# Optimization experiments

Measured on AMD Instinct MI355X. Metric: run time of the kernel, lower is better.

Reference implementation:

```python
import jax, jax.numpy as jnp
import numpy as np

EMBED_DIM = 1024
NUM_HEADS = 16
HEAD_DIM = EMBED_DIM // NUM_HEADS
NUM_FEATS = 256
YAT_EPS = 0.1
BATCH = 4
SEQ = 4096


def setup_inputs() -> dict:
    key = jax.random.key(0)
    ks = jax.random.split(key, 6)
    s = 1.0 / np.sqrt(EMBED_DIM)
    return {
        "x": jax.random.normal(ks[0], (BATCH, SEQ, EMBED_DIM), jnp.float32),
        "Wq": jax.random.normal(ks[1], (EMBED_DIM, EMBED_DIM), jnp.float32) * s,
        "bq": jnp.zeros((EMBED_DIM,), jnp.float32),
        "Wk": jax.random.normal(ks[2], (EMBED_DIM, EMBED_DIM), jnp.float32) * s,
        "bk": jnp.zeros((EMBED_DIM,), jnp.float32),
        "Wv": jax.random.normal(ks[3], (EMBED_DIM, EMBED_DIM), jnp.float32) * s,
        "bv": jnp.zeros((EMBED_DIM,), jnp.float32),
        "Wo": jax.random.normal(ks[4], (EMBED_DIM, EMBED_DIM), jnp.float32) * s,
        "bo": jnp.zeros((EMBED_DIM,), jnp.float32),
        "projection": jax.random.normal(ks[5], (NUM_HEADS, NUM_FEATS, HEAD_DIM), jnp.float32),
    }


def _spherical_features(x, projection):
    # x: (b, h, s, d) -> (b, h, s, f)
    x_norm = x / (jnp.linalg.norm(x, axis=-1, keepdims=True) + 1e-8)
    proj = jnp.einsum('bhsd,hfd->bhsf', x_norm, projection)
    return jax.nn.relu(proj) + YAT_EPS


def reference(x, Wq, bq, Wk, bk, Wv, bv, Wo, bo, projection):
    b, s, _ = x.shape
    def heads(t):
        return jnp.transpose(t.reshape(b, s, NUM_HEADS, HEAD_DIM), (0, 2, 1, 3))
    Q = heads(x @ Wq + bq)
    K = heads(x @ Wk + bk)
    V = heads(x @ Wv + bv)
    Qp = _spherical_features(Q, projection)  # (b,h,s,f)
    Kp = _spherical_features(K, projection)
    KV = jnp.einsum('bhsf,bhsd->bhfd', Kp, V)           # (b,h,f,d)
    QKV = jnp.einsum('bhsf,bhfd->bhsd', Qp, KV)          # (b,h,s,d)
    K_sum = jnp.sum(Kp, axis=2)                          # (b,h,f)
    normalizer = jnp.einsum('bhsf,bhf->bhs', Qp, K_sum)[..., None]
    normalizer = jnp.maximum(normalizer, 1e-6)
    out = QKV / normalizer
    out = jnp.transpose(out, (0, 2, 1, 3)).reshape(b, s, EMBED_DIM)
    return out @ Wo + bo
```

## Files before the change

### kernel.cpp

```cpp
#include <hip/hip_runtime.h>
#include <stdint.h>

typedef __bf16 bf16_t;
typedef __bf16 bf16x4 __attribute__((ext_vector_type(4)));
typedef __bf16 bf16x8 __attribute__((ext_vector_type(8)));
typedef float  f32x4  __attribute__((ext_vector_type(4)));

typedef __attribute__((address_space(1))) const uint32_t gas_u32;
typedef __attribute__((address_space(3))) uint32_t las_u32;

#define MFMA16(a, b, c) __builtin_amdgcn_mfma_f32_16x16x32_bf16((a), (b), (c), 0, 0, 0)
#define SBAR() __builtin_amdgcn_s_barrier()
#define WAIT_LGKM0() asm volatile("s_waitcnt lgkmcnt(0)")

__device__ __forceinline__ void gl_lds16(const bf16_t* g, bf16_t* l) {
    __builtin_amdgcn_global_load_lds((gas_u32*)g, (las_u32*)l, 16, 0, 0);
}

__global__ __launch_bounds__(256) void castbf(const float* __restrict__ X,
                                              bf16_t* __restrict__ Xb)
{
    size_t i = ((size_t)blockIdx.x * 256 + threadIdx.x) * 8;
    float4 a = *(const float4*)&X[i];
    float4 b = *(const float4*)&X[i + 4];
    bf16x8 o;
    o[0] = (bf16_t)a.x; o[1] = (bf16_t)a.y; o[2] = (bf16_t)a.z; o[3] = (bf16_t)a.w;
    o[4] = (bf16_t)b.x; o[5] = (bf16_t)b.y; o[6] = (bf16_t)b.z; o[7] = (bf16_t)b.w;
    *(bf16x8*)&Xb[i] = o;
}

__global__ __launch_bounds__(256) void ktrans(
    const float* __restrict__ W0, const float* __restrict__ W1,
    const float* __restrict__ W2, const float* __restrict__ W3,
    bf16_t* __restrict__ WT)
{
    __shared__ float t[64 * 68];
    const int z = blockIdx.z;
    const float* W = (z == 0) ? W0 : (z == 1) ? W1 : (z == 2) ? W2 : W3;
    bf16_t* O = WT + (size_t)z * 1024 * 1024;
    const int r0 = blockIdx.y * 64, c0 = blockIdx.x * 64;
    const int tid = threadIdx.x;
    const int row = tid >> 2, colg = (tid & 3) * 16;
#pragma unroll
    for (int p = 0; p < 4; ++p)
        *(float4*)&t[row * 68 + colg + p * 4] =
            *(const float4*)&W[(size_t)(r0 + row) * 1024 + c0 + colg + p * 4];
    __syncthreads();
    bf16x8 v0, v1;
#pragma unroll
    for (int j = 0; j < 8; ++j) {
        v0[j] = (bf16_t)t[(colg + j) * 68 + row];
        v1[j] = (bf16_t)t[(colg + 8 + j) * 68 + row];
    }
    *(bf16x8*)&O[(size_t)(c0 + row) * 1024 + r0 + colg] = v0;
    *(bf16x8*)&O[(size_t)(c0 + row) * 1024 + r0 + colg + 8] = v1;
}

template <int CMODE, typename OutT>
__global__ __launch_bounds__(512, 2) void gemm256(
    const bf16_t* __restrict__ A, const bf16_t* __restrict__ Bt,
    const float* __restrict__ b0, const float* __restrict__ b1,
    const float* __restrict__ b2, OutT* __restrict__ C,
    int M, int N, int K)
{
    __shared__ bf16_t lds[2][2][256 * 64];
    const int tid = threadIdx.x;
    const int lane = tid & 63, wave = tid >> 6;
    const int q = lane >> 4, ln = lane & 15;
    const int m0 = blockIdx.x * 256, n0 = blockIdx.y * 256;
    const int wm = (wave >> 2) * 128, wn = (wave & 3) * 64;
    const int NT = K >> 6;

    const bf16_t* Ag = A + (size_t)m0 * K;
    const bf16_t* Bg = Bt + (size_t)n0 * K;

    const bf16_t* gstage[4][2];
    bf16_t* lstage[4][2];
#pragma unroll
    for (int cs = 0; cs < 4; ++cs) {
        const int mat = cs >> 1, half = cs & 1;
#pragma unroll
        for (int r = 0; r < 2; ++r) {
            int idx = r * 512 + tid;
            int ri = idx >> 3;
            int row = mat ? (half * 32 + (ri & 31) + ((ri & ~31) << 1))
                          : (half * 64 + (ri & 63) + ((ri & 64) << 1));
            int gs = (idx & 7) ^ (row & 7);
            gstage[cs][r] = (mat ? Bg : Ag) + (size_t)row * K + gs * 8;
            lstage[cs][r] = &lds[0][mat][row * 64 + (idx & 7) * 8];
        }
    }
    auto stage = [&](int cs, int tt) {
        const int koff = tt << 6;
        const int bsel = (tt & 1) << 15;
#pragma unroll
        for (int r = 0; r < 2; ++r)
            gl_lds16(gstage[cs][r] + koff, lstage[cs][r] + bsel);
    };

    int aoff[2][4][2], boff[2][2][2];
#pragma unroll
    for (int mh = 0; mh < 2; ++mh)
#pragma unroll
        for (int mf = 0; mf < 4; ++mf)
#pragma unroll
            for (int ks = 0; ks < 2; ++ks) {
                int row = wm + (mh * 4 + mf) * 16 + ln;
                int g = ((ks << 2) + q) ^ (row & 7);
                aoff[mh][mf][ks] = row * 64 + g * 8;
            }
#pragma unroll
    for (int nh = 0; nh < 2; ++nh)
#pragma unroll
        for (int nf = 0; nf < 2; ++nf)
#pragma unroll
            for (int ks = 0; ks < 2; ++ks) {
                int row = wn + (nh * 2 + nf) * 16 + ln;
                int g = ((ks << 2) + q) ^ (row & 7);
                boff[nh][nf][ks] = row * 64 + g * 8;
            }
    bf16_t* ldsA = &lds[0][0][0];
    bf16_t* ldsB = &lds[0][1][0];

    bf16x8 aL[4][2], bL0[2][2], bL1[2][2];
    auto lda = [&](int mh, int cur) {
        const int b = cur << 15;
#pragma unroll
        for (int mf = 0; mf < 4; ++mf)
#pragma unroll
            for (int ks = 0; ks < 2; ++ks)
                aL[mf][ks] = *(const bf16x8*)&ldsA[b + aoff[mh][mf][ks]];
    };
    auto ldb = [&](bf16x8 (&bL)[2][2], int nh, int cur) {
        const int b = cur << 15;
#pragma unroll
        for (int nf = 0; nf < 2; ++nf)
#pragma unroll
            for (int ks = 0; ks < 2; ++ks)
                bL[nf][ks] = *(const bf16x8*)&ldsB[b + boff[nh][nf][ks]];
    };

    f32x4 acc[8][4] = {};
    auto mm = [&](bf16x8 (&bL)[2][2], int mh, int nh) {
        __builtin_amdgcn_s_setprio(1);
#pragma unroll
        for (int mf = 0; mf < 4; ++mf)
#pragma unroll
            for (int nf = 0; nf < 2; ++nf)
#pragma unroll
                for (int ks = 0; ks < 2; ++ks)
                    acc[mh * 4 + mf][nh * 2 + nf] =
                        MFMA16(aL[mf][ks], bL[nf][ks], acc[mh * 4 + mf][nh * 2 + nf]);
        __builtin_amdgcn_s_setprio(0);
    };

    stage(0, 0); stage(2, 0); stage(3, 0); stage(1, 0);
    stage(0, 1); stage(2, 1); stage(3, 1);
    asm volatile("s_waitcnt vmcnt(6)");
    __builtin_amdgcn_sched_barrier(0);
    SBAR();

    for (int t = 0; t < NT; ++t) {
        const int cur = t & 1;
        lda(0, cur); ldb(bL0, 0, cur);
        if (t + 1 < NT) stage(1, t + 1);
        SBAR(); WAIT_LGKM0();
        mm(bL0, 0, 0);
        SBAR();
        ldb(bL1, 1, cur);
        if (t + 2 < NT) stage(0, t + 2);
        SBAR(); WAIT_LGKM0();
        mm(bL1, 0, 1);
        SBAR();
        lda(1, cur);
        if (t + 2 < NT) stage(2, t + 2);
        SBAR(); WAIT_LGKM0();
        mm(bL0, 1, 0);
        SBAR();
        if (t + 2 < NT) stage(3, t + 2);
        SBAR();
        mm(bL1, 1, 1);
        if (t + 2 < NT) asm volatile("s_waitcnt vmcnt(6)");
        else            asm volatile("s_waitcnt vmcnt(0)");
        __builtin_amdgcn_sched_barrier(0);
        SBAR();
    }
    __syncthreads();

    if (CMODE == 0) {
        float* myCf = (float*)&lds[0][0][0] + wave * 1088;
        const int nf0 = n0 + wn;
        const int mfst = m0 + wm;
#pragma unroll
        for (int mt = 0; mt < 8; ++mt) {
#pragma unroll
            for (int nt = 0; nt < 4; ++nt) {
                float bv = b0[nf0 + nt * 16 + ln];
#pragma unroll
                for (int r = 0; r < 4; ++r)
                    myCf[(q * 4 + r) * 68 + nt * 16 + ln] = acc[mt][nt][r] + bv;
            }
#pragma unroll
            for (int c = 0; c < 4; ++c) {
                int flat = c * 64 + lane;
                int rr = flat >> 4, co = (flat & 15) * 4;
                f32x4 v = *(const f32x4*)&myCf[rr * 68 + co];
                *(f32x4*)&C[(size_t)(mfst + mt * 16 + rr) * N + nf0 + co] = v;
            }
        }
    } else {
        bf16_t* myCs = &lds[0][0][0] + wave * 2304;
        const int n_first = n0 + wn;
        const int t_ = n_first >> 10;
        const int h = (n_first >> 6) & 15;
        const float* bp = (t_ == 0) ? b0 : (t_ == 1) ? b1 : b2;
        const int m_first = m0 + wm;
        const int bI = m_first >> 12, s0 = m_first & 4095;
        bf16_t* Cp = (bf16_t*)C + (size_t)t_ * 16777216 + (size_t)(bI * 16 + h) * 262144;
#pragma unroll
        for (int p = 0; p < 4; ++p) {
#pragma unroll
            for (int mh2 = 0; mh2 < 2; ++mh2) {
                int mf = p * 2 + mh2;
#pragma unroll
                for (int nt = 0; nt < 4; ++nt) {
                    float bv = bp[(n_first + nt * 16 + ln) & 1023];
#pragma unroll
                    for (int r = 0; r < 4; ++r)
                        myCs[(mh2 * 16 + q * 4 + r) * 72 + nt * 16 + ln] =
                            (bf16_t)(acc[mf][nt][r] + bv);
                }
            }
#pragma unroll
            for (int c = 0; c < 4; ++c) {
                int flat = c * 64 + lane;
                int rr = flat >> 3, co = (flat & 7) * 8;
                bf16x8 v = *(const bf16x8*)&myCs[rr * 72 + co];
                *(bf16x8*)&Cp[(size_t)(s0 + p * 32 + rr) * 64 + co] = v;
            }
            __syncthreads();
        }
    }
}

__global__ __launch_bounds__(256) void kside(
    const bf16_t* __restrict__ Khm, const bf16_t* __restrict__ Vhm,
    const bf16_t* __restrict__ proj, float* __restrict__ P)
{
    __shared__ bf16_t KpT[256 * 72];
    __shared__ bf16_t Vt[80 * 72];
    const int tid = threadIdx.x;
    const int lane = tid & 63, wave = tid >> 6;
    const int q = lane >> 4, ln = lane & 15;
    const int bh = blockIdx.x, c = blockIdx.y;

    const bf16_t* Kh = Khm + (size_t)bh * 262144;
    const bf16_t* Vh = Vhm + (size_t)bh * 262144;
    const bf16_t* pr = proj + (size_t)(bh & 15) * 16384;

    for (int i = tid; i < 16 * 72; i += 256) {
        int rr = i / 72, cc = i % 72;
        Vt[(64 + rr) * 72 + cc] = (rr == 0) ? (bf16_t)1.0f : (bf16_t)0.0f;
    }
    bf16x8 pf[4][2];
#pragma unroll
    for (int nt = 0; nt < 4; ++nt)
#pragma unroll
        for (int ks = 0; ks < 2; ++ks)
            pf[nt][ks] = *(const bf16x8*)&pr[(size_t)(wave * 64 + nt * 16 + ln) * 64 + ks * 32 + q * 8];

    f32x4 kv[4][5] = {};
    const int s_base = c * 512;
    for (int st = 0; st < 8; ++st) {
        const int s0 = s_base + st * 64;
        f32x4 fa[4][4] = {};
#pragma unroll
        for (int mt = 0; mt < 4; ++mt) {
            const bf16_t* rp = &Kh[(size_t)(s0 + mt * 16 + ln) * 64 + q * 8];
            bf16x8 a0 = *(const bf16x8*)rp;
            bf16x8 a1 = *(const bf16x8*)(rp + 32);
            float f[16], ss = 0.f;
#pragma unroll
            for (int i = 0; i < 8; ++i) { f[i] = (float)a0[i]; f[8 + i] = (float)a1[i]; }
#pragma unroll
            for (int i = 0; i < 16; ++i) ss += f[i] * f[i];
            ss += __shfl_xor(ss, 16, 64);
            ss += __shfl_xor(ss, 32, 64);
            float sc = 1.0f / (sqrtf(ss) + 1e-8f);
            bf16x8 na0, na1;
#pragma unroll
            for (int i = 0; i < 8; ++i) {
                na0[i] = (bf16_t)(f[i] * sc);
                na1[i] = (bf16_t)(f[8 + i] * sc);
            }
#pragma unroll
            for (int nt = 0; nt < 4; ++nt) {
                fa[mt][nt] = MFMA16(na0, pf[nt][0], fa[mt][nt]);
                fa[mt][nt] = MFMA16(na1, pf[nt][1], fa[mt][nt]);
            }
        }
        __syncthreads();
#pragma unroll
        for (int mt = 0; mt < 4; ++mt)
#pragma unroll
            for (int nt = 0; nt < 4; ++nt) {
                bf16x4 kp;
#pragma unroll
                for (int r = 0; r < 4; ++r)
                    kp[r] = (bf16_t)(fmaxf(fa[mt][nt][r], 0.0f) + 0.1f);
                *(bf16x4*)&KpT[(wave * 64 + nt * 16 + ln) * 72 + mt * 16 + q * 4] = kp;
            }
        for (int j = tid; j < 512; j += 256) {
            int s = j >> 3, d0 = (j & 7) * 8;
            bf16x8 v = *(const bf16x8*)&Vh[(size_t)(s0 + s) * 64 + d0];
#pragma unroll
            for (int e = 0; e < 8; ++e) Vt[(d0 + e) * 72 + s] = v[e];
        }
        __syncthreads();
#pragma unroll
        for (int ks = 0; ks < 2; ++ks)
#pragma unroll
            for (int mt = 0; mt < 4; ++mt) {
                bf16x8 a = *(const bf16x8*)&KpT[(wave * 64 + mt * 16 + ln) * 72 + ks * 32 + q * 8];
#pragma unroll
                for (int nt = 0; nt < 5; ++nt) {
                    bf16x8 bb = *(const bf16x8*)&Vt[(nt * 16 + ln) * 72 + ks * 32 + q * 8];
                    kv[mt][nt] = MFMA16(a, bb, kv[mt][nt]);
                }
            }
    }
    float* Pp = P + (size_t)(bh * 8 + c) * 65 * 256;
#pragma unroll
    for (int mt = 0; mt < 4; ++mt)
#pragma unroll
        for (int nt = 0; nt < 5; ++nt)
            if (nt < 4 || ln == 0)
                *(f32x4*)&Pp[(size_t)(nt * 16 + ln) * 256 + wave * 64 + mt * 16 + q * 4] = kv[mt][nt];
}

__global__ __launch_bounds__(256) void kreduce(const float* __restrict__ P, bf16_t* __restrict__ KVt)
{
    size_t i = (size_t)blockIdx.x * 256 + threadIdx.x;
    int f = (int)(i & 255);
    int n = (int)((i >> 8) % 80);
    int bh = (int)(i / (256 * 80));
    float s = 0.f;
    if (n < 65) {
        const float* p = P + (size_t)bh * 8 * 65 * 256 + (size_t)n * 256 + f;
#pragma unroll
        for (int c = 0; c < 8; ++c) s += p[(size_t)c * 65 * 256];
    }
    KVt[i] = (bf16_t)s;
}

__global__ __launch_bounds__(256) void qside(
    const bf16_t* __restrict__ Qhm, const bf16_t* __restrict__ proj,
    const bf16_t* __restrict__ KVt, bf16_t* __restrict__ attn)
{
    __shared__ bf16_t Qp[128 * 136];
    const int tid = threadIdx.x;
    const int lane = tid & 63, wave = tid >> 6;
    const int q = lane >> 4, ln = lane & 15;
    const int bh = blockIdx.x, stile = blockIdx.y;
    const int bI = bh >> 4, h = bh & 15;

    const bf16_t* Qh = Qhm + (size_t)bh * 262144 + (size_t)stile * 128 * 64;
    const bf16_t* pr = proj + (size_t)h * 16384;
    const bf16_t* kv = KVt + (size_t)bh * 20480;

    bf16x8 na[2][2];
#pragma unroll
    for (int mt = 0; mt < 2; ++mt) {
        const bf16_t* rp = &Qh[(size_t)(wave * 32 + mt * 16 + ln) * 64 + q * 8];
        bf16x8 a0 = *(const bf16x8*)rp;
        bf16x8 a1 = *(const bf16x8*)(rp + 32);
        float f[16], ss = 0.f;
#pragma unroll
        for (int i = 0; i < 8; ++i) { f[i] = (float)a0[i]; f[8 + i] = (float)a1[i]; }
#pragma unroll
        for (int i = 0; i < 16; ++i) ss += f[i] * f[i];
        ss += __shfl_xor(ss, 16, 64);
        ss += __shfl_xor(ss, 32, 64);
        float sc = 1.0f / (sqrtf(ss) + 1e-8f);
#pragma unroll
        for (int i = 0; i < 8; ++i) {
            na[mt][0][i] = (bf16_t)(f[i] * sc);
            na[mt][1][i] = (bf16_t)(f[8 + i] * sc);
        }
    }

    f32x4 oacc[2][5] = {};
#pragma unroll
    for (int fh = 0; fh < 2; ++fh) {
        f32x4 fa[2][8] = {};
#pragma unroll
        for (int ks = 0; ks < 2; ++ks) {
            bf16x8 bb[8];
#pragma unroll
            for (int nt = 0; nt < 8; ++nt)
                bb[nt] = *(const bf16x8*)&pr[(size_t)(fh * 128 + nt * 16 + ln) * 64 + ks * 32 + q * 8];
#pragma unroll
            for (int mt = 0; mt < 2; ++mt)
#pragma unroll
                for (int nt = 0; nt < 8; ++nt)
                    fa[mt][nt] = MFMA16(na[mt][ks], bb[nt], fa[mt][nt]);
        }
#pragma unroll
        for (int mt = 0; mt < 2; ++mt)
#pragma unroll
            for (int nt = 0; nt < 8; ++nt)
#pragma unroll
                for (int r = 0; r < 4; ++r)
                    Qp[(wave * 32 + mt * 16 + q * 4 + r) * 136 + nt * 16 + ln] =
                        (bf16_t)(fmaxf(fa[mt][nt][r], 0.0f) + 0.1f);
#pragma unroll
        for (int ks = 0; ks < 4; ++ks) {
            bf16x8 aa[2];
#pragma unroll
            for (int mt = 0; mt < 2; ++mt)
                aa[mt] = *(const bf16x8*)&Qp[(wave * 32 + mt * 16 + ln) * 136 + ks * 32 + q * 8];
#pragma unroll
            for (int nt = 0; nt < 5; ++nt) {
                bf16x8 bb = *(const bf16x8*)&kv[(size_t)(nt * 16 + ln) * 256 + fh * 128 + ks * 32 + q * 8];
#pragma unroll
                for (int mt = 0; mt < 2; ++mt)
                    oacc[mt][nt] = MFMA16(aa[mt], bb, oacc[mt][nt]);
            }
        }
    }
    bf16_t* Ap = attn + ((size_t)(bI * 4096 + stile * 128) * 1024) + h * 64;
#pragma unroll
    for (int mt = 0; mt < 2; ++mt)
#pragma unroll
        for (int r = 0; r < 4; ++r) {
            float nrm = fmaxf(__shfl(oacc[mt][4][r], lane & 48, 64), 1e-6f);
            int sl = wave * 32 + mt * 16 + q * 4 + r;
#pragma unroll
            for (int nt = 0; nt < 4; ++nt)
                Ap[(size_t)sl * 1024 + nt * 16 + ln] = (bf16_t)(oacc[mt][nt][r] / nrm);
        }
}

extern "C" void kernel_launch(void* const* d_in, const int* in_sizes, int n_in,
                              void* d_out, int out_size, void* d_ws, size_t ws_size,
                              hipStream_t stream)
{
    const float* x = (const float*)d_in[0];
    const float* Wq = (const float*)d_in[1];
    const float* bq = (const float*)d_in[2];
    const float* Wk = (const float*)d_in[3];
    const float* bk = (const float*)d_in[4];
    const float* Wv = (const float*)d_in[5];
    const float* bv = (const float*)d_in[6];
    const float* Wo = (const float*)d_in[7];
    const float* bo = (const float*)d_in[8];
    const float* proj = (const float*)d_in[9];

    char* ws = (char*)d_ws;
    bf16_t* WT = (bf16_t*)(ws);
    bf16_t* projb = (bf16_t*)(ws + (8ull << 20));
    bf16_t* KVt = (bf16_t*)(ws + (9ull << 20));
    bf16_t* Q = (bf16_t*)(ws + (12ull << 20));
    bf16_t* K = (bf16_t*)(ws + (44ull << 20));
    bf16_t* V = (bf16_t*)(ws + (76ull << 20));
    bf16_t* xb = (bf16_t*)(ws + (108ull << 20));
    float* P = (float*)xb;
    bf16_t* attn = V;
    float* out = (float*)d_out;

    castbf<<<8192, 256, 0, stream>>>(x, xb);
    castbf<<<128, 256, 0, stream>>>(proj, projb);
    ktrans<<<dim3(16, 16, 4), 256, 0, stream>>>(Wq, Wk, Wv, Wo, WT);
    gemm256<2, bf16_t><<<dim3(64, 12), 512, 0, stream>>>(
        xb, WT, bq, bk, bv, Q, 16384, 3072, 1024);
    kside<<<dim3(64, 8), 256, 0, stream>>>(K, V, projb, P);
    kreduce<<<5120, 256, 0, stream>>>(P, KVt);
    qside<<<dim3(64, 32), 256, 0, stream>>>(Q, projb, KVt, attn);
    gemm256<0, float><<<dim3(64, 4), 512, 0, stream>>>(
        attn, WT + 3ull * 1048576, bo, bo, bo, out, 16384, 1024, 1024);
}
```

Baseline: 411.0 us.

## Double-buffer GEMM register fragments and cut barriers in main loop

The GEMM main loop now keeps two A fragment sets and two B fragment sets in registers, so the next tile's LDS reads are issued before the last MFMA quadrant of the current tile. The number of s_barriers per iteration drops from eight to three, and the explicit lgkmcnt waits are removed in favour of compiler-inserted waits. Bias pointer parameters are renamed to avoid clashing with the new fragment names. This is meant to overlap LDS reads with MFMA work and cut synchronisation stalls. It costs more VGPRs under the 512-thread, 2-block launch bounds and relies on the remaining barriers to protect the double-buffered LDS.

New measurement: 413.6 us. Within noise of the previous version (+0.6%).

```diff
diff --git a/kernel.cpp b/kernel.cpp
--- a/kernel.cpp
+++ b/kernel.cpp
@@ -10,8 +10,7 @@
 typedef __attribute__((address_space(3))) uint32_t las_u32;
 
 #define MFMA16(a, b, c) __builtin_amdgcn_mfma_f32_16x16x32_bf16((a), (b), (c), 0, 0, 0)
-#define SBAR() __builtin_amdgcn_s_barrier()
-#define WAIT_LGKM0() asm volatile("s_waitcnt lgkmcnt(0)")
+#define SBARM() asm volatile("s_barrier" ::: "memory")
 
 __device__ __forceinline__ void gl_lds16(const bf16_t* g, bf16_t* l) {
     __builtin_amdgcn_global_load_lds((gas_u32*)g, (las_u32*)l, 16, 0, 0);
@@ -59,8 +58,8 @@
 template <int CMODE, typename OutT>
 __global__ __launch_bounds__(512, 2) void gemm256(
     const bf16_t* __restrict__ A, const bf16_t* __restrict__ Bt,
-    const float* __restrict__ b0, const float* __restrict__ b1,
-    const float* __restrict__ b2, OutT* __restrict__ C,
+    const float* __restrict__ b0v, const float* __restrict__ b1v,
+    const float* __restrict__ b2v, OutT* __restrict__ C,
     int M, int N, int K)
 {
     __shared__ bf16_t lds[2][2][256 * 64];
@@ -122,26 +121,26 @@
     bf16_t* ldsA = &lds[0][0][0];
     bf16_t* ldsB = &lds[0][1][0];
 
-    bf16x8 aL[4][2], bL0[2][2], bL1[2][2];
-    auto lda = [&](int mh, int cur) {
+    bf16x8 aA[4][2], aB[4][2], b0f[2][2], b1f[2][2];
+    auto lda = [&](bf16x8 (&d)[4][2], int mh, int cur) {
         const int b = cur << 15;
 #pragma unroll
         for (int mf = 0; mf < 4; ++mf)
 #pragma unroll
             for (int ks = 0; ks < 2; ++ks)
-                aL[mf][ks] = *(const bf16x8*)&ldsA[b + aoff[mh][mf][ks]];
+                d[mf][ks] = *(const bf16x8*)&ldsA[b + aoff[mh][mf][ks]];
     };
-    auto ldb = [&](bf16x8 (&bL)[2][2], int nh, int cur) {
+    auto ldb = [&](bf16x8 (&d)[2][2], int nh, int cur) {
         const int b = cur << 15;
 #pragma unroll
         for (int nf = 0; nf < 2; ++nf)
 #pragma unroll
             for (int ks = 0; ks < 2; ++ks)
-                bL[nf][ks] = *(const bf16x8*)&ldsB[b + boff[nh][nf][ks]];
+                d[nf][ks] = *(const bf16x8*)&ldsB[b + boff[nh][nf][ks]];
     };
 
     f32x4 acc[8][4] = {};
-    auto mm = [&](bf16x8 (&bL)[2][2], int mh, int nh) {
+    auto mm = [&](bf16x8 (&a)[4][2], bf16x8 (&b)[2][2], int mh, int nh) {
         __builtin_amdgcn_s_setprio(1);
 #pragma unroll
         for (int mf = 0; mf < 4; ++mf)
@@ -150,40 +149,33 @@
 #pragma unroll
                 for (int ks = 0; ks < 2; ++ks)
                     acc[mh * 4 + mf][nh * 2 + nf] =
-                        MFMA16(aL[mf][ks], bL[nf][ks], acc[mh * 4 + mf][nh * 2 + nf]);
+                        MFMA16(a[mf][ks], b[nf][ks], acc[mh * 4 + mf][nh * 2 + nf]);
         __builtin_amdgcn_s_setprio(0);
     };
 
     stage(0, 0); stage(2, 0); stage(3, 0); stage(1, 0);
     stage(0, 1); stage(2, 1); stage(3, 1);
-    asm volatile("s_waitcnt vmcnt(6)");
-    __builtin_amdgcn_sched_barrier(0);
-    SBAR();
+    asm volatile("s_waitcnt vmcnt(6)" ::: "memory");
+    SBARM();
+    lda(aA, 0, 0); ldb(b0f, 0, 0);
 
     for (int t = 0; t < NT; ++t) {
-        const int cur = t & 1;
-        lda(0, cur); ldb(bL0, 0, cur);
+        const int cur = t & 1, nxt = cur ^ 1;
+        ldb(b1f, 1, cur);
         if (t + 1 < NT) stage(1, t + 1);
-        SBAR(); WAIT_LGKM0();
-        mm(bL0, 0, 0);
-        SBAR();
-        ldb(bL1, 1, cur);
+        mm(aA, b0f, 0, 0);
+        SBARM();
+        lda(aB, 1, cur);
         if (t + 2 < NT) stage(0, t + 2);
-        SBAR(); WAIT_LGKM0();
-        mm(bL1, 0, 1);
-        SBAR();
-        lda(1, cur);
-        if (t + 2 < NT) stage(2, t + 2);
-        SBAR(); WAIT_LGKM0();
-        mm(bL0, 1, 0);
-        SBAR();
-        if (t + 2 < NT) stage(3, t + 2);
-        SBAR();
-        mm(bL1, 1, 1);
-        if (t + 2 < NT) asm volatile("s_waitcnt vmcnt(6)");
-        else            asm volatile("s_waitcnt vmcnt(0)");
-        __builtin_amdgcn_sched_barrier(0);
-        SBAR();
+        mm(aA, b1f, 0, 1);
+        SBARM();
+        if (t + 2 < NT) { stage(2, t + 2); stage(3, t + 2); }
+        mm(aB, b0f, 1, 0);
+        if (t + 2 < NT) asm volatile("s_waitcnt vmcnt(6)" ::: "memory");
+        else            asm volatile("s_waitcnt vmcnt(0)" ::: "memory");
+        if (t + 1 < NT) { lda(aA, 0, nxt); ldb(b0f, 0, nxt); }
+        mm(aB, b1f, 1, 1);
+        SBARM();
     }
     __syncthreads();
 
@@ -195,7 +187,7 @@
         for (int mt = 0; mt < 8; ++mt) {
 #pragma unroll
             for (int nt = 0; nt < 4; ++nt) {
-                float bv = b0[nf0 + nt * 16 + ln];
+                float bv = b0v[nf0 + nt * 16 + ln];
 #pragma unroll
                 for (int r = 0; r < 4; ++r)
                     myCf[(q * 4 + r) * 68 + nt * 16 + ln] = acc[mt][nt][r] + bv;
@@ -213,7 +205,7 @@
         const int n_first = n0 + wn;
         const int t_ = n_first >> 10;
         const int h = (n_first >> 6) & 15;
-        const float* bp = (t_ == 0) ? b0 : (t_ == 1) ? b1 : b2;
+        const float* bp = (t_ == 0) ? b0v : (t_ == 1) ? b1v : b2v;
         const int m_first = m0 + wm;
         const int bI = m_first >> 12, s0 = m_first & 4095;
         bf16_t* Cp = (bf16_t*)C + (size_t)t_ * 16777216 + (size_t)(bI * 16 + h) * 262144;
```
